# Optimization experiments

Measured on AMD Instinct MI355X. Metric: run time of the kernel, lower is better.

## Reference

```python
import jax, jax.numpy as jnp
import numpy as np

N = 50000      # n_nodes
E = 800000     # n_edges
F_IN = 128     # raw feature dim
H = 64         # hidden_channels
L = 2          # max_hash_hops / num GCN layers
NUM_PERM = 128 # minhash permutations
HLL_M = 64     # 2**hll_p registers


def setup_inputs() -> dict:
    key = jax.random.key(0)
    ks = jax.random.split(key, 8)
    x = jax.random.normal(ks[0], (N, F_IN), jnp.float32)
    edge_index = jax.random.randint(ks[1], (2, E), 0, N, dtype=jnp.int32)
    minhash0 = jax.random.randint(ks[2], (N, NUM_PERM), 0, 2147483647, dtype=jnp.int32)
    hll0 = jax.random.randint(ks[3], (N, HLL_M), 0, 20, dtype=jnp.int32)
    W_enc = jax.random.normal(ks[4], (F_IN, H), jnp.float32) / np.sqrt(F_IN)
    b_enc = jnp.zeros((H,), jnp.float32)
    W_convs = jax.random.normal(ks[5], (L, H, H), jnp.float32) / np.sqrt(H)
    b_convs = jnp.zeros((L, H), jnp.float32)
    return {"x": x, "edge_index": edge_index, "minhash0": minhash0, "hll0": hll0,
            "W_enc": W_enc, "b_enc": b_enc, "W_convs": W_convs, "b_convs": b_convs}


def _hll_count(hll):
    # standard HyperLogLog estimator: alpha_m * m^2 / sum(2^-reg)
    m = hll.shape[1]
    alpha = 0.7213 / (1.0 + 1.079 / m)
    s = jnp.sum(jnp.exp2(-hll.astype(jnp.float32)), axis=1)  # [N]
    return alpha * m * m / s


def reference(x, edge_index, minhash0, hll0, W_enc, b_enc, W_convs, b_convs):
    src, dst = edge_index[0], edge_index[1]
    loops = jnp.arange(N, dtype=src.dtype)
    # add_self_loops: used for both hash propagation and (internally) by GCNConv
    src_sl = jnp.concatenate([src, loops])  # [E+N]
    dst_sl = jnp.concatenate([dst, loops])

    # gcn_norm: D^-1/2 (A+I) D^-1/2 with degrees counted on self-looped graph
    deg = jax.ops.segment_sum(jnp.ones_like(dst_sl, jnp.float32), dst_sl, num_segments=N)
    dis = jnp.where(deg > 0, jax.lax.rsqrt(jnp.maximum(deg, 1.0)), 0.0)
    norm = dis[src_sl] * dis[dst_sl]  # [E+N]

    # k=0: feature encoder (dropout off in eval)
    h = x @ W_enc + b_enc  # [N, H]

    mh, hll = minhash0, hll0
    cards = []
    for k in range(L):
        # hash propagation: HLL = register-wise max over neighborhood,
        # minhash = permutation-wise min over neighborhood (self-looped graph)
        hll = jax.ops.segment_max(hll[src_sl], dst_sl, num_segments=N)
        mh = jax.ops.segment_min(mh[src_sl], dst_sl, num_segments=N)
        cards.append(_hll_count(hll))
        # GCNConv: gather - (x W) - scatter with symmetric norm, then residual
        msg = (h @ W_convs[k])[src_sl] * norm[:, None]  # [E+N, H]
        out = jax.ops.segment_sum(msg, dst_sl, num_segments=N) + b_convs[k]
        h = h + out  # feature_prop == 'residual' (dropout off)

    cards = jnp.stack(cards, axis=1)  # [N, L]
    return h, cards, mh, hll
```

## Files before the change

kernel.cpp:

```cpp
#include <hip/hip_runtime.h>
#include <hip/hip_bf16.h>

typedef unsigned int uint;
typedef unsigned short ushort;

#define N_NODES 50000
#define N_EDGES 800000
#define FDIM 128
#define HID 64
#define NPERM 128
#define HLLM 64

#define BSHIFT 8
#define BNODES 256
#define NBUCK 196
#define SCAT_BLOCKS 256
#define EDGES_PER_BLK 3125
#define HIST_BLOCKS 64
#define EDGES_PER_HIST 12500
#define MH_BLOCKS 12500
#define HLL_BLOCKS 3125
#define SLICE_CAP 6400
#define CONV_BLOCKS 782


__device__ __forceinline__ void mh_body(int node, int l, const int* __restrict__ offsets,
                                        const ushort* __restrict__ csr,
                                        const uint* __restrict__ mh_in,
                                        uint* __restrict__ out_p, float* __restrict__ out_f) {
    int s = offsets[node], e = offsets[node + 1];
    uint mn0 = 0xFFFFu, mn1 = 0xFFFFu, mn2 = 0xFFFFu, mn3 = 0xFFFFu;
    for (int p = s; p < e; p += 8) {
        int q1 = p + 1, q2 = p + 2, q3 = p + 3, q4 = p + 4, q5 = p + 5, q6 = p + 6, q7 = p + 7;
        uint j0 = csr[p];
        uint j1 = csr[q1 < e ? q1 : p];
        uint j2 = csr[q2 < e ? q2 : p];
        uint j3 = csr[q3 < e ? q3 : p];
        uint j4 = csr[q4 < e ? q4 : p];
        uint j5 = csr[q5 < e ? q5 : p];
        uint j6 = csr[q6 < e ? q6 : p];
        uint j7 = csr[q7 < e ? q7 : p];
        uint a0 = mh_in[(size_t)j0 * 64 + l];
        uint a1 = mh_in[(size_t)j1 * 64 + l];
        uint a2 = mh_in[(size_t)j2 * 64 + l];
        uint a3 = mh_in[(size_t)j3 * 64 + l];
        uint a4 = mh_in[(size_t)j4 * 64 + l];
        uint a5 = mh_in[(size_t)j5 * 64 + l];
        uint a6 = mh_in[(size_t)j6 * 64 + l];
        uint a7 = mh_in[(size_t)j7 * 64 + l];
        mn0 = min(mn0, min(a0 & 0xFFFFu, a1 & 0xFFFFu));
        mn1 = min(mn1, min(a0 >> 16, a1 >> 16));
        mn2 = min(mn2, min(a2 & 0xFFFFu, a3 & 0xFFFFu));
        mn3 = min(mn3, min(a2 >> 16, a3 >> 16));
        mn0 = min(mn0, min(a4 & 0xFFFFu, a5 & 0xFFFFu));
        mn1 = min(mn1, min(a4 >> 16, a5 >> 16));
        mn2 = min(mn2, min(a6 & 0xFFFFu, a7 & 0xFFFFu));
        mn3 = min(mn3, min(a6 >> 16, a7 >> 16));
    }
    mn0 = min(mn0, mn2); mn1 = min(mn1, mn3);
    if (out_p) {
        out_p[(size_t)node * 64 + l] = mn0 | (mn1 << 16);
    } else {
        float2 w;
        w.x = __uint_as_float(mn0 << 16);
        w.y = __uint_as_float(mn1 << 16);
        *(float2*)(out_f + (size_t)node * NPERM + 2 * l) = w;
    }
}

__device__ __forceinline__ void hll_body(int node, int q, const int* __restrict__ offsets,
                                         const ushort* __restrict__ csr,
                                         const uint* __restrict__ hll_in,
                                         uint* __restrict__ out_p, float* __restrict__ out_f,
                                         float* __restrict__ cards, int kcol) {
    int s = offsets[node], e = offsets[node + 1];
    uint m0 = 0, m1 = 0, m2 = 0, m3 = 0;
#define HLL_ACC(vv) do { uint _v = (vv); \
        m0 = max(m0, _v & 0xFFu); m1 = max(m1, (_v >> 8) & 0xFFu); \
        m2 = max(m2, (_v >> 16) & 0xFFu); m3 = max(m3, _v >> 24); } while (0)
    for (int p = s; p < e; p += 8) {
        int q1 = p + 1, q2 = p + 2, q3 = p + 3, q4 = p + 4, q5 = p + 5, q6 = p + 6, q7 = p + 7;
        uint j0 = csr[p];
        uint j1 = csr[q1 < e ? q1 : p];
        uint j2 = csr[q2 < e ? q2 : p];
        uint j3 = csr[q3 < e ? q3 : p];
        uint j4 = csr[q4 < e ? q4 : p];
        uint j5 = csr[q5 < e ? q5 : p];
        uint j6 = csr[q6 < e ? q6 : p];
        uint j7 = csr[q7 < e ? q7 : p];
        uint a0 = hll_in[(size_t)j0 * 16 + q];
        uint a1 = hll_in[(size_t)j1 * 16 + q];
        uint a2 = hll_in[(size_t)j2 * 16 + q];
        uint a3 = hll_in[(size_t)j3 * 16 + q];
        uint a4 = hll_in[(size_t)j4 * 16 + q];
        uint a5 = hll_in[(size_t)j5 * 16 + q];
        uint a6 = hll_in[(size_t)j6 * 16 + q];
        uint a7 = hll_in[(size_t)j7 * 16 + q];
        HLL_ACC(a0); HLL_ACC(a1); HLL_ACC(a2); HLL_ACC(a3);
        HLL_ACC(a4); HLL_ACC(a5); HLL_ACC(a6); HLL_ACC(a7);
    }
#undef HLL_ACC
    if (out_p) out_p[(size_t)node * 16 + q] = m0 | (m1 << 8) | (m2 << 16) | (m3 << 24);
    if (out_f) {
        float4 w = {(float)m0, (float)m1, (float)m2, (float)m3};
        *(float4*)(out_f + (size_t)node * HLLM + 4 * q) = w;
    }
    float v = exp2f(-(float)m0) + exp2f(-(float)m1) + exp2f(-(float)m2) + exp2f(-(float)m3);
    v += __shfl_xor(v, 1); v += __shfl_xor(v, 2);
    v += __shfl_xor(v, 4); v += __shfl_xor(v, 8);
    if (q == 0) {
        const float alphamm = (float)(0.7213 / (1.0 + 1.079 / 64.0) * 64.0 * 64.0);
        cards[(size_t)node * 2 + kcol] = alphamm / v;
    }
}

__device__ __forceinline__ void agg_body(int node, int c, const int* __restrict__ offsets,
                                         const ushort* __restrict__ csr,
                                         const ushort* __restrict__ hWs,
                                         const float* __restrict__ dis,
                                         const float* __restrict__ b,
                                         const float* __restrict__ h_in,
                                         float* __restrict__ h_out) {
    int s = offsets[node], e = offsets[node + 1];
    float acc0 = 0.f, acc1 = 0.f;
    for (int p = s; p < e; p += 8) {
        int q1 = p + 1, q2 = p + 2, q3 = p + 3, q4 = p + 4, q5 = p + 5, q6 = p + 6, q7 = p + 7;
        bool v1 = q1 < e, v2 = q2 < e, v3 = q3 < e, v4 = q4 < e, v5 = q5 < e, v6 = q6 < e, v7 = q7 < e;
        uint j0 = csr[p];
        uint j1 = csr[v1 ? q1 : p];
        uint j2 = csr[v2 ? q2 : p];
        uint j3 = csr[v3 ? q3 : p];
        uint j4 = csr[v4 ? q4 : p];
        uint j5 = csr[v5 ? q5 : p];
        uint j6 = csr[v6 ? q6 : p];
        uint j7 = csr[v7 ? q7 : p];
        uint a0 = hWs[(size_t)j0 * HID + c];
        uint a1 = hWs[(size_t)j1 * HID + c];
        uint a2 = hWs[(size_t)j2 * HID + c];
        uint a3 = hWs[(size_t)j3 * HID + c];
        uint a4 = hWs[(size_t)j4 * HID + c];
        uint a5 = hWs[(size_t)j5 * HID + c];
        uint a6 = hWs[(size_t)j6 * HID + c];
        uint a7 = hWs[(size_t)j7 * HID + c];
        acc0 += __uint_as_float(a0 << 16);
        acc0 += v1 ? __uint_as_float(a1 << 16) : 0.f;
        acc1 += v2 ? __uint_as_float(a2 << 16) : 0.f;
        acc1 += v3 ? __uint_as_float(a3 << 16) : 0.f;
        acc0 += v4 ? __uint_as_float(a4 << 16) : 0.f;
        acc0 += v5 ? __uint_as_float(a5 << 16) : 0.f;
        acc1 += v6 ? __uint_as_float(a6 << 16) : 0.f;
        acc1 += v7 ? __uint_as_float(a7 << 16) : 0.f;
    }
    float acc = acc0 + acc1;
    h_out[(size_t)node * HID + c] = h_in[(size_t)node * HID + c] + b[c] + dis[node] * acc;
}

__device__ __forceinline__ void convmm_body(int row, int c0, const float* __restrict__ h,
                                            const float* __restrict__ Ws,
                                            const float* __restrict__ dis,
                                            ushort* __restrict__ hWs) {
    float acc[16] = {0.f, 0.f, 0.f, 0.f, 0.f, 0.f, 0.f, 0.f,
                     0.f, 0.f, 0.f, 0.f, 0.f, 0.f, 0.f, 0.f};
    const float4* hr = (const float4*)(h + (size_t)row * HID);
    for (int k4 = 0; k4 < HID / 4; ++k4) {
        float4 hv = hr[k4];
        const float* wr = Ws + (k4 * 4) * HID + c0;
#pragma unroll
        for (int j = 0; j < 16; ++j) acc[j] = fmaf(hv.x, wr[j], acc[j]);
#pragma unroll
        for (int j = 0; j < 16; ++j) acc[j] = fmaf(hv.y, wr[HID + j], acc[j]);
#pragma unroll
        for (int j = 0; j < 16; ++j) acc[j] = fmaf(hv.z, wr[2 * HID + j], acc[j]);
#pragma unroll
        for (int j = 0; j < 16; ++j) acc[j] = fmaf(hv.w, wr[3 * HID + j], acc[j]);
    }
    float d = dis[row];
    ushort* o = hWs + (size_t)row * HID + c0;
#pragma unroll
    for (int j = 0; j < 16; ++j) {
        __hip_bfloat16 t = __float2bfloat16(d * acc[j]);
        o[j] = *(ushort*)&t;
    }
}


__global__ void __launch_bounds__(256) k_prep(const float* __restrict__ x,
                       const float* __restrict__ W_enc, const float* __restrict__ b_enc,
                       float* __restrict__ h,
                       const int* __restrict__ mh, uint* __restrict__ mhp,
                       const int* __restrict__ hll, uint* __restrict__ hp,
                       const int* __restrict__ dst, int* __restrict__ hist2d) {
    __shared__ float smem[FDIM * HID];
    int b = blockIdx.x;
    if (b < CONV_BLOCKS) {
        for (int idx = threadIdx.x; idx < FDIM * HID; idx += 256) smem[idx] = W_enc[idx];
        __syncthreads();
        int row = b * 64 + (threadIdx.x >> 2);
        int c0 = (threadIdx.x & 3) * 16;
        if (row >= N_NODES) return;
        float acc[16];
#pragma unroll
        for (int j = 0; j < 16; ++j) acc[j] = b_enc[c0 + j];
        const float4* xr = (const float4*)(x + (size_t)row * FDIM);
        for (int k4 = 0; k4 < FDIM / 4; ++k4) {
            float4 xv = xr[k4];
            const float* wr = smem + (k4 * 4) * HID + c0;
#pragma unroll
            for (int j = 0; j < 16; ++j) acc[j] = fmaf(xv.x, wr[j], acc[j]);
#pragma unroll
            for (int j = 0; j < 16; ++j) acc[j] = fmaf(xv.y, wr[HID + j], acc[j]);
#pragma unroll
            for (int j = 0; j < 16; ++j) acc[j] = fmaf(xv.z, wr[2 * HID + j], acc[j]);
#pragma unroll
            for (int j = 0; j < 16; ++j) acc[j] = fmaf(xv.w, wr[3 * HID + j], acc[j]);
        }
        float* hr = h + (size_t)row * HID + c0;
#pragma unroll
        for (int j = 0; j < 16; ++j) hr[j] = acc[j];
    } else if (b < CONV_BLOCKS + MH_BLOCKS) {
        int i = (b - CONV_BLOCKS) * 256 + threadIdx.x;
        int2 v = ((const int2*)mh)[i];
        uint u0 = __float_as_uint((float)v.x) >> 16;
        uint u1 = __float_as_uint((float)v.y) >> 16;
        mhp[i] = u0 | (u1 << 16);
    } else if (b < CONV_BLOCKS + MH_BLOCKS + HLL_BLOCKS) {
        int i = (b - CONV_BLOCKS - MH_BLOCKS) * 256 + threadIdx.x;
        int4 v = ((const int4*)hll)[i];
        hp[i] = (uint)v.x | ((uint)v.y << 8) | ((uint)v.z << 16) | ((uint)v.w << 24);
    } else {
        int hb = b - CONV_BLOCKS - MH_BLOCKS - HLL_BLOCKS;
        int* hsh = (int*)smem;
        for (int i = threadIdx.x; i < NBUCK; i += 256) hsh[i] = 0;
        __syncthreads();
        int e0 = hb * EDGES_PER_HIST;
        for (int i = threadIdx.x; i < EDGES_PER_HIST; i += 256)
            atomicAdd(&hsh[dst[e0 + i] >> BSHIFT], 1);
        __syncthreads();
        for (int i = threadIdx.x; i < NBUCK; i += 256)
            hist2d[hb * NBUCK + i] = hsh[i];
    }
}

__global__ void k_bktscan(const int* __restrict__ hist2d, int* __restrict__ bktcnt,
                          int* __restrict__ gbase, int* __restrict__ gcur,
                          int* __restrict__ offsets) {
    __shared__ int s[256];
    int t = threadIdx.x;
    int v = 0;
    if (t < NBUCK)
        for (int k = 0; k < HIST_BLOCKS; ++k) v += hist2d[k * NBUCK + t];
    s[t] = v;
    __syncthreads();
    for (int off = 1; off < 256; off <<= 1) {
        int u = (t >= off) ? s[t - off] : 0;
        __syncthreads();
        s[t] += u;
        __syncthreads();
    }
    if (t < NBUCK) {
        int ex = s[t] - v;
        bktcnt[t] = v; gbase[t] = ex; gcur[t] = ex;
    }
    if (t == 0) offsets[N_NODES] = N_EDGES + N_NODES;
}


__global__ void __launch_bounds__(256) k_scatter(const int* __restrict__ src,
                          const int* __restrict__ dst,
                          int* __restrict__ gcur, uint* __restrict__ ebuf) {
    __shared__ uint ecache[EDGES_PER_BLK];
    __shared__ int cnt[NBUCK];
    __shared__ int cur[NBUCK];
    int t = threadIdx.x;
    for (int i = t; i < NBUCK; i += 256) cnt[i] = 0;
    __syncthreads();
    int e0 = blockIdx.x * EDGES_PER_BLK;
    for (int i = t; i < EDGES_PER_BLK; i += 256) {
        int d = dst[e0 + i];
        int s = src[e0 + i];
        ecache[i] = ((uint)s << 16) | (uint)d;
        atomicAdd(&cnt[d >> BSHIFT], 1);
    }
    __syncthreads();
    for (int b = t; b < NBUCK; b += 256)
        cur[b] = atomicAdd(&gcur[b], cnt[b]);
    __syncthreads();
    for (int i = t; i < EDGES_PER_BLK; i += 256) {
        uint en = ecache[i];
        uint d = en & 0xFFFFu;
        int p = atomicAdd(&cur[d >> BSHIFT], 1);
        ebuf[p] = ((en >> 16) << BSHIFT) | (d & (BNODES - 1));
    }
}


__global__ void __launch_bounds__(256) k_csr(const uint* __restrict__ ebuf,
                      const int* __restrict__ gbase, const int* __restrict__ bktcnt,
                      int* __restrict__ offsets, float* __restrict__ dis,
                      ushort* __restrict__ csr) {
    __shared__ int lcur[BNODES];
    __shared__ int ssum[256];
    __shared__ uint slice[SLICE_CAP];
    int b = blockIdx.x;
    int lo = b << BSHIFT;
    int nbkt = min(BNODES, N_NODES - lo);
    int ebase = gbase[b];
    int ecnt = bktcnt[b];
    int t = threadIdx.x;
    lcur[t] = 0;
    __syncthreads();
    for (int i = t; i < ecnt; i += 256)
        atomicAdd(&lcur[ebuf[ebase + i] & (BNODES - 1)], 1);
    __syncthreads();
    int a0 = lcur[t];
    ssum[t] = a0;
    __syncthreads();
    for (int off = 1; off < 256; off <<= 1) {
        int u = (t >= off) ? ssum[t - off] : 0;
        __syncthreads();
        ssum[t] += u;
        __syncthreads();
    }
    int pre = ssum[t] - a0;
    if (t < nbkt) {
        int st = pre + t;
        slice[st] = (uint)(lo + t);
        lcur[t] = st + 1;
        offsets[lo + t] = ebase + lo + st;
        dis[lo + t] = rsqrtf((float)(a0 + 1));
    }
    __syncthreads();
    for (int i = t; i < ecnt; i += 256) {
        uint en = ebuf[ebase + i];
        int p = atomicAdd(&lcur[en & (BNODES - 1)], 1);
        slice[p] = en >> BSHIFT;
    }
    __syncthreads();
    int slen = ecnt + nbkt;
    int gb = ebase + lo;
    for (int i = t; i < slen; i += 256) csr[gb + i] = (ushort)slice[i];
}


__global__ void __launch_bounds__(256) k_hopA(const int* __restrict__ offsets,
                    const ushort* __restrict__ csr,
                    const uint* __restrict__ mh_in, uint* __restrict__ mh_out_p,
                    const uint* __restrict__ hll_in, uint* __restrict__ hll_out_p,
                    float* __restrict__ cards,
                    const float* __restrict__ h, const float* __restrict__ W,
                    const float* __restrict__ dis, ushort* __restrict__ hWs) {
    __shared__ float Ws[HID * HID];
    int blk = blockIdx.x;
    if (blk < MH_BLOCKS) {
        int node = blk * 4 + (threadIdx.x >> 6);
        mh_body(node, threadIdx.x & 63, offsets, csr, mh_in, mh_out_p, nullptr);
    } else if (blk < MH_BLOCKS + HLL_BLOCKS) {
        int node = (blk - MH_BLOCKS) * 16 + (threadIdx.x >> 4);
        hll_body(node, threadIdx.x & 15, offsets, csr, hll_in, hll_out_p, nullptr, cards, 0);
    } else {
        for (int i = threadIdx.x; i < HID * HID; i += 256) Ws[i] = W[i];
        __syncthreads();
        int row = (blk - MH_BLOCKS - HLL_BLOCKS) * 64 + (threadIdx.x >> 2);
        if (row >= N_NODES) return;
        convmm_body(row, (threadIdx.x & 3) * 16, h, Ws, dis, hWs);
    }
}


__global__ void __launch_bounds__(256) k_hopB(const int* __restrict__ offsets,
                    const ushort* __restrict__ csr,
                    const uint* __restrict__ mh_in, float* __restrict__ mh_out_f,
                    const ushort* __restrict__ hWs, const float* __restrict__ b0,
                    float* __restrict__ h_cur,
                    const uint* __restrict__ hll_in, float* __restrict__ hll_out_f,
                    float* __restrict__ cards, const float* __restrict__ dis) {
    int blk = blockIdx.x;
    if (blk < MH_BLOCKS) {
        int node = blk * 4 + (threadIdx.x >> 6);
        mh_body(node, threadIdx.x & 63, offsets, csr, mh_in, nullptr, mh_out_f);
    } else if (blk < 2 * MH_BLOCKS) {
        int node = (blk - MH_BLOCKS) * 4 + (threadIdx.x >> 6);
        agg_body(node, threadIdx.x & 63, offsets, csr, hWs, dis, b0, h_cur, h_cur);
    } else {
        int node = (blk - 2 * MH_BLOCKS) * 16 + (threadIdx.x >> 4);
        hll_body(node, threadIdx.x & 15, offsets, csr, hll_in, nullptr, hll_out_f, cards, 1);
    }
}


__global__ void __launch_bounds__(256) k_conv(const float* __restrict__ h,
                         const float* __restrict__ W, const float* __restrict__ dis,
                         ushort* __restrict__ hWs) {
    __shared__ float Ws[HID * HID];
    for (int i = threadIdx.x; i < HID * HID; i += 256) Ws[i] = W[i];
    __syncthreads();
    int row = blockIdx.x * 64 + (threadIdx.x >> 2);
    if (row >= N_NODES) return;
    convmm_body(row, (threadIdx.x & 3) * 16, h, Ws, dis, hWs);
}


__global__ void __launch_bounds__(256) k_agg(const int* __restrict__ offsets,
                      const ushort* __restrict__ csr, const ushort* __restrict__ hWs,
                      const float* __restrict__ dis, const float* __restrict__ b,
                      const float* __restrict__ h_in, float* __restrict__ h_out) {
    int node = blockIdx.x * 4 + (threadIdx.x >> 6);
    agg_body(node, threadIdx.x & 63, offsets, csr, hWs, dis, b, h_in, h_out);
}


static inline char* align256(char* p) {
    return (char*)(((uintptr_t)p + 255) & ~(uintptr_t)255);
}

extern "C" void kernel_launch(void* const* d_in, const int* in_sizes, int n_in,
                              void* d_out, int out_size, void* d_ws, size_t ws_size,
                              hipStream_t stream) {
    const float* x       = (const float*)d_in[0];
    const int*   ei      = (const int*)d_in[1];
    const int*   mh0     = (const int*)d_in[2];
    const int*   hll0    = (const int*)d_in[3];
    const float* W_enc   = (const float*)d_in[4];
    const float* b_enc   = (const float*)d_in[5];
    const float* W_convs = (const float*)d_in[6];
    const float* b_convs = (const float*)d_in[7];

    float* out       = (float*)d_out;
    float* out_h     = out;
    float* out_cards = out + (size_t)N_NODES * HID;
    float* out_mh    = out_cards + (size_t)N_NODES * 2;
    float* out_hll   = out_mh + (size_t)N_NODES * NPERM;

    char* w = (char*)d_ws;
    int*   hist2d  = (int*)w;   w = align256(w + (size_t)HIST_BLOCKS * NBUCK * 4);
    int*   bktcnt  = (int*)w;   w = align256(w + (size_t)NBUCK * 4);
    int*   gbase   = (int*)w;   w = align256(w + (size_t)NBUCK * 4);
    int*   gcur    = (int*)w;   w = align256(w + (size_t)NBUCK * 4);
    int*   offsets = (int*)w;   w = align256(w + (size_t)(N_NODES + 1) * 4);
    float* dis     = (float*)w; w = align256(w + (size_t)N_NODES * 4);
    ushort* csr    = (ushort*)w; w = align256(w + (size_t)(N_EDGES + N_NODES) * 2);
    uint*  mhp0    = (uint*)w;  w = align256(w + (size_t)N_NODES * 64 * 4);
    uint*  mhA     = (uint*)w;  w = align256(w + (size_t)N_NODES * 64 * 4);
    uint*  hp0     = (uint*)w;  w = align256(w + (size_t)N_NODES * 16 * 4);
    uint*  hllA    = (uint*)w;  w = align256(w + (size_t)N_NODES * 16 * 4);
    float* h_cur   = (float*)w; w = align256(w + (size_t)N_NODES * HID * 4);
    ushort* hWs    = (ushort*)w; w = align256(w + (size_t)N_NODES * HID * 2);
    uint*  ebuf    = mhA;

    const int* src = ei;
    const int* dst = ei + N_EDGES;

    k_prep<<<CONV_BLOCKS + MH_BLOCKS + HLL_BLOCKS + HIST_BLOCKS, 256, 0, stream>>>(
        x, W_enc, b_enc, h_cur, mh0, mhp0, hll0, hp0, dst, hist2d);
    k_bktscan<<<1, 256, 0, stream>>>(hist2d, bktcnt, gbase, gcur, offsets);
    k_scatter<<<SCAT_BLOCKS, 256, 0, stream>>>(src, dst, gcur, ebuf);
    k_csr<<<NBUCK, 256, 0, stream>>>(ebuf, gbase, bktcnt, offsets, dis, csr);

    k_hopA<<<MH_BLOCKS + HLL_BLOCKS + CONV_BLOCKS, 256, 0, stream>>>(
        offsets, csr, mhp0, mhA, hp0, hllA, out_cards, h_cur, W_convs, dis, hWs);
    k_hopB<<<2 * MH_BLOCKS + HLL_BLOCKS, 256, 0, stream>>>(
        offsets, csr, mhA, out_mh, hWs, b_convs, h_cur, hllA, out_hll, out_cards, dis);
    k_conv<<<CONV_BLOCKS, 256, 0, stream>>>(h_cur, W_convs + HID * HID, dis, hWs);
    k_agg<<<MH_BLOCKS, 256, 0, stream>>>(offsets, csr, hWs, dis, b_convs + HID, h_cur, out_h);
}
```

Measured before the change: 215.6 us.

## Pad CSR rows to multiples of eight with dummy node for vector index loads

```diff
diff --git a/kernel.cpp b/kernel.cpp
--- a/kernel.cpp
+++ b/kernel.cpp
@@ -10,6 +10,7 @@
 #define HID 64
 #define NPERM 128
 #define HLLM 64
+#define DUMMY 50000
 
 #define BSHIFT 8
 #define BNODES 256
@@ -20,44 +21,43 @@
 #define EDGES_PER_HIST 12500
 #define MH_BLOCKS 12500
 #define HLL_BLOCKS 3125
-#define SLICE_CAP 6400
+#define SLICE_CAP 8448
 #define CONV_BLOCKS 782
 
-
-__device__ __forceinline__ void mh_body(int node, int l, const int* __restrict__ offsets,
+__device__ __forceinline__ uint pk_min_u16(uint a, uint b) {
+    uint d;
+    asm("v_pk_min_u16 %0, %1, %2" : "=v"(d) : "v"(a), "v"(b));
+    return d;
+}
+
+
+__device__ __forceinline__ void mh_body(int node, uint l, const int2* __restrict__ off2,
                                         const ushort* __restrict__ csr,
                                         const uint* __restrict__ mh_in,
                                         uint* __restrict__ out_p, float* __restrict__ out_f) {
-    int s = offsets[node], e = offsets[node + 1];
-    uint mn0 = 0xFFFFu, mn1 = 0xFFFFu, mn2 = 0xFFFFu, mn3 = 0xFFFFu;
-    for (int p = s; p < e; p += 8) {
-        int q1 = p + 1, q2 = p + 2, q3 = p + 3, q4 = p + 4, q5 = p + 5, q6 = p + 6, q7 = p + 7;
-        uint j0 = csr[p];
-        uint j1 = csr[q1 < e ? q1 : p];
-        uint j2 = csr[q2 < e ? q2 : p];
-        uint j3 = csr[q3 < e ? q3 : p];
-        uint j4 = csr[q4 < e ? q4 : p];
-        uint j5 = csr[q5 < e ? q5 : p];
-        uint j6 = csr[q6 < e ? q6 : p];
-        uint j7 = csr[q7 < e ? q7 : p];
-        uint a0 = mh_in[(size_t)j0 * 64 + l];
-        uint a1 = mh_in[(size_t)j1 * 64 + l];
-        uint a2 = mh_in[(size_t)j2 * 64 + l];
-        uint a3 = mh_in[(size_t)j3 * 64 + l];
-        uint a4 = mh_in[(size_t)j4 * 64 + l];
-        uint a5 = mh_in[(size_t)j5 * 64 + l];
-        uint a6 = mh_in[(size_t)j6 * 64 + l];
-        uint a7 = mh_in[(size_t)j7 * 64 + l];
-        mn0 = min(mn0, min(a0 & 0xFFFFu, a1 & 0xFFFFu));
-        mn1 = min(mn1, min(a0 >> 16, a1 >> 16));
-        mn2 = min(mn2, min(a2 & 0xFFFFu, a3 & 0xFFFFu));
-        mn3 = min(mn3, min(a2 >> 16, a3 >> 16));
-        mn0 = min(mn0, min(a4 & 0xFFFFu, a5 & 0xFFFFu));
-        mn1 = min(mn1, min(a4 >> 16, a5 >> 16));
-        mn2 = min(mn2, min(a6 & 0xFFFFu, a7 & 0xFFFFu));
-        mn3 = min(mn3, min(a6 >> 16, a7 >> 16));
-    }
-    mn0 = min(mn0, mn2); mn1 = min(mn1, mn3);
+    int2 se = off2[node];
+    uint mnA = 0xFFFFFFFFu, mnB = 0xFFFFFFFFu, mnC = 0xFFFFFFFFu, mnD = 0xFFFFFFFFu;
+    for (int p = se.x; p < se.y; p += 8) {
+        uint4 c4 = *(const uint4*)(csr + p);
+        uint j0 = c4.x & 0xFFFFu, j1 = c4.x >> 16;
+        uint j2 = c4.y & 0xFFFFu, j3 = c4.y >> 16;
+        uint j4 = c4.z & 0xFFFFu, j5 = c4.z >> 16;
+        uint j6 = c4.w & 0xFFFFu, j7 = c4.w >> 16;
+        uint a0 = mh_in[j0 * 64u + l];
+        uint a1 = mh_in[j1 * 64u + l];
+        uint a2 = mh_in[j2 * 64u + l];
+        uint a3 = mh_in[j3 * 64u + l];
+        uint a4 = mh_in[j4 * 64u + l];
+        uint a5 = mh_in[j5 * 64u + l];
+        uint a6 = mh_in[j6 * 64u + l];
+        uint a7 = mh_in[j7 * 64u + l];
+        mnA = pk_min_u16(mnA, a0); mnB = pk_min_u16(mnB, a1);
+        mnC = pk_min_u16(mnC, a2); mnD = pk_min_u16(mnD, a3);
+        mnA = pk_min_u16(mnA, a4); mnB = pk_min_u16(mnB, a5);
+        mnC = pk_min_u16(mnC, a6); mnD = pk_min_u16(mnD, a7);
+    }
+    mnA = pk_min_u16(pk_min_u16(mnA, mnB), pk_min_u16(mnC, mnD));
+    uint mn0 = mnA & 0xFFFFu, mn1 = mnA >> 16;
     if (out_p) {
         out_p[(size_t)node * 64 + l] = mn0 | (mn1 << 16);
     } else {
@@ -68,34 +68,30 @@
     }
 }
 
-__device__ __forceinline__ void hll_body(int node, int q, const int* __restrict__ offsets,
+__device__ __forceinline__ void hll_body(int node, uint q, const int2* __restrict__ off2,
                                          const ushort* __restrict__ csr,
                                          const uint* __restrict__ hll_in,
                                          uint* __restrict__ out_p, float* __restrict__ out_f,
                                          float* __restrict__ cards, int kcol) {
-    int s = offsets[node], e = offsets[node + 1];
+    int2 se = off2[node];
     uint m0 = 0, m1 = 0, m2 = 0, m3 = 0;
 #define HLL_ACC(vv) do { uint _v = (vv); \
         m0 = max(m0, _v & 0xFFu); m1 = max(m1, (_v >> 8) & 0xFFu); \
         m2 = max(m2, (_v >> 16) & 0xFFu); m3 = max(m3, _v >> 24); } while (0)
-    for (int p = s; p < e; p += 8) {
-        int q1 = p + 1, q2 = p + 2, q3 = p + 3, q4 = p + 4, q5 = p + 5, q6 = p + 6, q7 = p + 7;
-        uint j0 = csr[p];
-        uint j1 = csr[q1 < e ? q1 : p];
-        uint j2 = csr[q2 < e ? q2 : p];
-        uint j3 = csr[q3 < e ? q3 : p];
-        uint j4 = csr[q4 < e ? q4 : p];
-        uint j5 = csr[q5 < e ? q5 : p];
-        uint j6 = csr[q6 < e ? q6 : p];
-        uint j7 = csr[q7 < e ? q7 : p];
-        uint a0 = hll_in[(size_t)j0 * 16 + q];
-        uint a1 = hll_in[(size_t)j1 * 16 + q];
-        uint a2 = hll_in[(size_t)j2 * 16 + q];
-        uint a3 = hll_in[(size_t)j3 * 16 + q];
-        uint a4 = hll_in[(size_t)j4 * 16 + q];
-        uint a5 = hll_in[(size_t)j5 * 16 + q];
-        uint a6 = hll_in[(size_t)j6 * 16 + q];
-        uint a7 = hll_in[(size_t)j7 * 16 + q];
+    for (int p = se.x; p < se.y; p += 8) {
+        uint4 c4 = *(const uint4*)(csr + p);
+        uint j0 = c4.x & 0xFFFFu, j1 = c4.x >> 16;
+        uint j2 = c4.y & 0xFFFFu, j3 = c4.y >> 16;
+        uint j4 = c4.z & 0xFFFFu, j5 = c4.z >> 16;
+        uint j6 = c4.w & 0xFFFFu, j7 = c4.w >> 16;
+        uint a0 = hll_in[j0 * 16u + q];
+        uint a1 = hll_in[j1 * 16u + q];
+        uint a2 = hll_in[j2 * 16u + q];
+        uint a3 = hll_in[j3 * 16u + q];
+        uint a4 = hll_in[j4 * 16u + q];
+        uint a5 = hll_in[j5 * 16u + q];
+        uint a6 = hll_in[j6 * 16u + q];
+        uint a7 = hll_in[j7 * 16u + q];
         HLL_ACC(a0); HLL_ACC(a1); HLL_ACC(a2); HLL_ACC(a3);
         HLL_ACC(a4); HLL_ACC(a5); HLL_ACC(a6); HLL_ACC(a7);
     }
@@ -114,42 +110,33 @@
     }
 }
 
-__device__ __forceinline__ void agg_body(int node, int c, const int* __restrict__ offsets,
+__device__ __forceinline__ void agg_body(int node, uint c, const int2* __restrict__ off2,
                                          const ushort* __restrict__ csr,
                                          const ushort* __restrict__ hWs,
                                          const float* __restrict__ dis,
                                          const float* __restrict__ b,
                                          const float* __restrict__ h_in,
                                          float* __restrict__ h_out) {
-    int s = offsets[node], e = offsets[node + 1];
+    int2 se = off2[node];
     float acc0 = 0.f, acc1 = 0.f;
-    for (int p = s; p < e; p += 8) {
-        int q1 = p + 1, q2 = p + 2, q3 = p + 3, q4 = p + 4, q5 = p + 5, q6 = p + 6, q7 = p + 7;
-        bool v1 = q1 < e, v2 = q2 < e, v3 = q3 < e, v4 = q4 < e, v5 = q5 < e, v6 = q6 < e, v7 = q7 < e;
-        uint j0 = csr[p];
-        uint j1 = csr[v1 ? q1 : p];
-        uint j2 = csr[v2 ? q2 : p];
-        uint j3 = csr[v3 ? q3 : p];
-        uint j4 = csr[v4 ? q4 : p];
-        uint j5 = csr[v5 ? q5 : p];
-        uint j6 = csr[v6 ? q6 : p];
-        uint j7 = csr[v7 ? q7 : p];
-        uint a0 = hWs[(size_t)j0 * HID + c];
-        uint a1 = hWs[(size_t)j1 * HID + c];
-        uint a2 = hWs[(size_t)j2 * HID + c];
-        uint a3 = hWs[(size_t)j3 * HID + c];
-        uint a4 = hWs[(size_t)j4 * HID + c];
-        uint a5 = hWs[(size_t)j5 * HID + c];
-        uint a6 = hWs[(size_t)j6 * HID + c];
-        uint a7 = hWs[(size_t)j7 * HID + c];
-        acc0 += __uint_as_float(a0 << 16);
-        acc0 += v1 ? __uint_as_float(a1 << 16) : 0.f;
-        acc1 += v2 ? __uint_as_float(a2 << 16) : 0.f;
-        acc1 += v3 ? __uint_as_float(a3 << 16) : 0.f;
-        acc0 += v4 ? __uint_as_float(a4 << 16) : 0.f;
-        acc0 += v5 ? __uint_as_float(a5 << 16) : 0.f;
-        acc1 += v6 ? __uint_as_float(a6 << 16) : 0.f;
-        acc1 += v7 ? __uint_as_float(a7 << 16) : 0.f;
+    for (int p = se.x; p < se.y; p += 8) {
+        uint4 c4 = *(const uint4*)(csr + p);
+        uint j0 = c4.x & 0xFFFFu, j1 = c4.x >> 16;
+        uint j2 = c4.y & 0xFFFFu, j3 = c4.y >> 16;
+        uint j4 = c4.z & 0xFFFFu, j5 = c4.z >> 16;
+        uint j6 = c4.w & 0xFFFFu, j7 = c4.w >> 16;
+        uint a0 = hWs[j0 * 64u + c];
+        uint a1 = hWs[j1 * 64u + c];
+        uint a2 = hWs[j2 * 64u + c];
+        uint a3 = hWs[j3 * 64u + c];
+        uint a4 = hWs[j4 * 64u + c];
+        uint a5 = hWs[j5 * 64u + c];
+        uint a6 = hWs[j6 * 64u + c];
+        uint a7 = hWs[j7 * 64u + c];
+        acc0 += __uint_as_float(a0 << 16) + __uint_as_float(a1 << 16)
+              + __uint_as_float(a2 << 16) + __uint_as_float(a3 << 16);
+        acc1 += __uint_as_float(a4 << 16) + __uint_as_float(a5 << 16)
+              + __uint_as_float(a6 << 16) + __uint_as_float(a7 << 16);
     }
     float acc = acc0 + acc1;
     h_out[(size_t)node * HID + c] = h_in[(size_t)node * HID + c] + b[c] + dis[node] * acc;
@@ -187,8 +174,8 @@
 __global__ void __launch_bounds__(256) k_prep(const float* __restrict__ x,
                        const float* __restrict__ W_enc, const float* __restrict__ b_enc,
                        float* __restrict__ h,
-                       const int* __restrict__ mh, uint* __restrict__ mhp,
-                       const int* __restrict__ hll, uint* __restrict__ hp,
+                       const int* __restrict__ mh, uint* __restrict__ mhp, uint* __restrict__ mhA,
+                       const int* __restrict__ hll, uint* __restrict__ hp, uint* __restrict__ hllA,
                        const int* __restrict__ dst, int* __restrict__ hist2d) {
     __shared__ float smem[FDIM * HID];
     int b = blockIdx.x;
@@ -227,7 +214,7 @@
         int i = (b - CONV_BLOCKS - MH_BLOCKS) * 256 + threadIdx.x;
         int4 v = ((const int4*)hll)[i];
         hp[i] = (uint)v.x | ((uint)v.y << 8) | ((uint)v.z << 16) | ((uint)v.w << 24);
-    } else {
+    } else if (b < CONV_BLOCKS + MH_BLOCKS + HLL_BLOCKS + HIST_BLOCKS) {
         int hb = b - CONV_BLOCKS - MH_BLOCKS - HLL_BLOCKS;
         int* hsh = (int*)smem;
         for (int i = threadIdx.x; i < NBUCK; i += 256) hsh[i] = 0;
@@ -238,12 +225,22 @@
         __syncthreads();
         for (int i = threadIdx.x; i < NBUCK; i += 256)
             hist2d[hb * NBUCK + i] = hsh[i];
+    } else {
+        int t = threadIdx.x;
+        if (t < 64) {
+            mhp[(size_t)DUMMY * 64 + t] = 0xFFFFFFFFu;
+            mhA[(size_t)DUMMY * 64 + t] = 0xFFFFFFFFu;
+        } else if (t < 80) {
+            hp[(size_t)DUMMY * 16 + (t - 64)] = 0u;
+        } else if (t < 96) {
+            hllA[(size_t)DUMMY * 16 + (t - 80)] = 0u;
+        }
     }
 }
 
 __global__ void k_bktscan(const int* __restrict__ hist2d, int* __restrict__ bktcnt,
                           int* __restrict__ gbase, int* __restrict__ gcur,
-                          int* __restrict__ offsets) {
+                          int* __restrict__ pcur) {
     __shared__ int s[256];
     int t = threadIdx.x;
     int v = 0;
@@ -261,7 +258,7 @@
         int ex = s[t] - v;
         bktcnt[t] = v; gbase[t] = ex; gcur[t] = ex;
     }
-    if (t == 0) offsets[N_NODES] = N_EDGES + N_NODES;
+    if (t == 0) pcur[0] = 0;
 }
 
 
@@ -296,11 +293,12 @@
 
 __global__ void __launch_bounds__(256) k_csr(const uint* __restrict__ ebuf,
                       const int* __restrict__ gbase, const int* __restrict__ bktcnt,
-                      int* __restrict__ offsets, float* __restrict__ dis,
-                      ushort* __restrict__ csr) {
+                      int* __restrict__ pcur, int2* __restrict__ off2,
+                      float* __restrict__ dis, ushort* __restrict__ csr) {
     __shared__ int lcur[BNODES];
     __shared__ int ssum[256];
     __shared__ uint slice[SLICE_CAP];
+    __shared__ int sbase;
     int b = blockIdx.x;
     int lo = b << BSHIFT;
     int nbkt = min(BNODES, N_NODES - lo);
@@ -313,7 +311,8 @@
         atomicAdd(&lcur[ebuf[ebase + i] & (BNODES - 1)], 1);
     __syncthreads();
     int a0 = lcur[t];
-    ssum[t] = a0;
+    int plen = (t < nbkt) ? ((a0 + 8) & ~7) : 0;
+    ssum[t] = plen;
     __syncthreads();
     for (int off = 1; off < 256; off <<= 1) {
         int u = (t >= off) ? ssum[t - off] : 0;
@@ -321,12 +320,14 @@
         ssum[t] += u;
         __syncthreads();
     }
-    int pre = ssum[t] - a0;
+    int ppre = ssum[t] - plen;
+    if (t == 255) sbase = atomicAdd(pcur, ssum[255]);
+    __syncthreads();
+    int base = sbase;
     if (t < nbkt) {
-        int st = pre + t;
-        slice[st] = (uint)(lo + t);
-        lcur[t] = st + 1;
-        offsets[lo + t] = ebase + lo + st;
+        slice[ppre] = (uint)(lo + t);
+        lcur[t] = ppre + 1;
+        off2[lo + t] = make_int2(base + ppre, base + ppre + plen);
         dis[lo + t] = rsqrtf((float)(a0 + 1));
     }
     __syncthreads();
@@ -336,13 +337,15 @@
         slice[p] = en >> BSHIFT;
     }
     __syncthreads();
-    int slen = ecnt + nbkt;
-    int gb = ebase + lo;
-    for (int i = t; i < slen; i += 256) csr[gb + i] = (ushort)slice[i];
-}
-
-
-__global__ void __launch_bounds__(256) k_hopA(const int* __restrict__ offsets,
+    if (t < nbkt)
+        for (int i = lcur[t]; i < ppre + plen; ++i) slice[i] = DUMMY;
+    __syncthreads();
+    int total = ssum[255];
+    for (int i = t; i < total; i += 256) csr[base + i] = (ushort)slice[i];
+}
+
+
+__global__ void __launch_bounds__(256) k_hopA(const int2* __restrict__ off2,
                     const ushort* __restrict__ csr,
                     const uint* __restrict__ mh_in, uint* __restrict__ mh_out_p,
                     const uint* __restrict__ hll_in, uint* __restrict__ hll_out_p,
@@ -353,21 +356,28 @@
     int blk = blockIdx.x;
     if (blk < MH_BLOCKS) {
         int node = blk * 4 + (threadIdx.x >> 6);
-        mh_body(node, threadIdx.x & 63, offsets, csr, mh_in, mh_out_p, nullptr);
+        mh_body(node, threadIdx.x & 63, off2, csr, mh_in, mh_out_p, nullptr);
     } else if (blk < MH_BLOCKS + HLL_BLOCKS) {
         int node = (blk - MH_BLOCKS) * 16 + (threadIdx.x >> 4);
-        hll_body(node, threadIdx.x & 15, offsets, csr, hll_in, hll_out_p, nullptr, cards, 0);
+        hll_body(node, threadIdx.x & 15, off2, csr, hll_in, hll_out_p, nullptr, cards, 0);
     } else {
         for (int i = threadIdx.x; i < HID * HID; i += 256) Ws[i] = W[i];
         __syncthreads();
         int row = (blk - MH_BLOCKS - HLL_BLOCKS) * 64 + (threadIdx.x >> 2);
-        if (row >= N_NODES) return;
-        convmm_body(row, (threadIdx.x & 3) * 16, h, Ws, dis, hWs);
-    }
-}
-
-
-__global__ void __launch_bounds__(256) k_hopB(const int* __restrict__ offsets,
+        int c0 = (threadIdx.x & 3) * 16;
+        if (row > N_NODES) return;
+        if (row == N_NODES) {
+            ushort* o = hWs + (size_t)row * HID + c0;
+#pragma unroll
+            for (int j = 0; j < 16; ++j) o[j] = 0;
+            return;
+        }
+        convmm_body(row, c0, h, Ws, dis, hWs);
+    }
+}
+
+
+__global__ void __launch_bounds__(256) k_hopB(const int2* __restrict__ off2,
                     const ushort* __restrict__ csr,
                     const uint* __restrict__ mh_in, float* __restrict__ mh_out_f,
                     const ushort* __restrict__ hWs, const float* __restrict__ b0,
@@ -377,13 +387,13 @@
     int blk = blockIdx.x;
     if (blk < MH_BLOCKS) {
         int node = blk * 4 + (threadIdx.x >> 6);
-        mh_body(node, threadIdx.x & 63, offsets, csr, mh_in, nullptr, mh_out_f);
+        mh_body(node, threadIdx.x & 63, off2, csr, mh_in, nullptr, mh_out_f);
     } else if (blk < 2 * MH_BLOCKS) {
         int node = (blk - MH_BLOCKS) * 4 + (threadIdx.x >> 6);
-        agg_body(node, threadIdx.x & 63, offsets, csr, hWs, dis, b0, h_cur, h_cur);
+        agg_body(node, threadIdx.x & 63, off2, csr, hWs, dis, b0, h_cur, h_cur);
     } else {
         int node = (blk - 2 * MH_BLOCKS) * 16 + (threadIdx.x >> 4);
-        hll_body(node, threadIdx.x & 15, offsets, csr, hll_in, nullptr, hll_out_f, cards, 1);
+        hll_body(node, threadIdx.x & 15, off2, csr, hll_in, nullptr, hll_out_f, cards, 1);
     }
 }
 
@@ -395,17 +405,24 @@
     for (int i = threadIdx.x; i < HID * HID; i += 256) Ws[i] = W[i];
     __syncthreads();
     int row = blockIdx.x * 64 + (threadIdx.x >> 2);
-    if (row >= N_NODES) return;
-    convmm_body(row, (threadIdx.x & 3) * 16, h, Ws, dis, hWs);
-}
-
-
-__global__ void __launch_bounds__(256) k_agg(const int* __restrict__ offsets,
+    int c0 = (threadIdx.x & 3) * 16;
+    if (row > N_NODES) return;
+    if (row == N_NODES) {
+        ushort* o = hWs + (size_t)row * HID + c0;
+#pragma unroll
+        for (int j = 0; j < 16; ++j) o[j] = 0;
+        return;
+    }
+    convmm_body(row, c0, h, Ws, dis, hWs);
+}
+
+
+__global__ void __launch_bounds__(256) k_agg(const int2* __restrict__ off2,
                       const ushort* __restrict__ csr, const ushort* __restrict__ hWs,
                       const float* __restrict__ dis, const float* __restrict__ b,
                       const float* __restrict__ h_in, float* __restrict__ h_out) {
     int node = blockIdx.x * 4 + (threadIdx.x >> 6);
-    agg_body(node, threadIdx.x & 63, offsets, csr, hWs, dis, b, h_in, h_out);
+    agg_body(node, threadIdx.x & 63, off2, csr, hWs, dis, b, h_in, h_out);
 }
 
 
@@ -436,30 +453,31 @@
     int*   bktcnt  = (int*)w;   w = align256(w + (size_t)NBUCK * 4);
     int*   gbase   = (int*)w;   w = align256(w + (size_t)NBUCK * 4);
     int*   gcur    = (int*)w;   w = align256(w + (size_t)NBUCK * 4);
-    int*   offsets = (int*)w;   w = align256(w + (size_t)(N_NODES + 1) * 4);
+    int*   pcur    = (int*)w;   w = align256(w + 4);
+    int2*  off2    = (int2*)w;  w = align256(w + (size_t)N_NODES * 8);
     float* dis     = (float*)w; w = align256(w + (size_t)N_NODES * 4);
-    ushort* csr    = (ushort*)w; w = align256(w + (size_t)(N_EDGES + N_NODES) * 2);
-    uint*  mhp0    = (uint*)w;  w = align256(w + (size_t)N_NODES * 64 * 4);
-    uint*  mhA     = (uint*)w;  w = align256(w + (size_t)N_NODES * 64 * 4);
-    uint*  hp0     = (uint*)w;  w = align256(w + (size_t)N_NODES * 16 * 4);
-    uint*  hllA    = (uint*)w;  w = align256(w + (size_t)N_NODES * 16 * 4);
+    ushort* csr    = (ushort*)w; w = align256(w + (size_t)(N_EDGES + 8 * N_NODES) * 2);
+    uint*  mhp0    = (uint*)w;  w = align256(w + (size_t)(N_NODES + 1) * 64 * 4);
+    uint*  mhA     = (uint*)w;  w = align256(w + (size_t)(N_NODES + 1) * 64 * 4);
+    uint*  hp0     = (uint*)w;  w = align256(w + (size_t)(N_NODES + 1) * 16 * 4);
+    uint*  hllA    = (uint*)w;  w = align256(w + (size_t)(N_NODES + 1) * 16 * 4);
     float* h_cur   = (float*)w; w = align256(w + (size_t)N_NODES * HID * 4);
-    ushort* hWs    = (ushort*)w; w = align256(w + (size_t)N_NODES * HID * 2);
+    ushort* hWs    = (ushort*)w; w = align256(w + (size_t)(N_NODES + 1) * HID * 2);
     uint*  ebuf    = mhA;
 
     const int* src = ei;
     const int* dst = ei + N_EDGES;
 
-    k_prep<<<CONV_BLOCKS + MH_BLOCKS + HLL_BLOCKS + HIST_BLOCKS, 256, 0, stream>>>(
-        x, W_enc, b_enc, h_cur, mh0, mhp0, hll0, hp0, dst, hist2d);
-    k_bktscan<<<1, 256, 0, stream>>>(hist2d, bktcnt, gbase, gcur, offsets);
+    k_prep<<<CONV_BLOCKS + MH_BLOCKS + HLL_BLOCKS + HIST_BLOCKS + 1, 256, 0, stream>>>(
+        x, W_enc, b_enc, h_cur, mh0, mhp0, mhA, hll0, hp0, hllA, dst, hist2d);
+    k_bktscan<<<1, 256, 0, stream>>>(hist2d, bktcnt, gbase, gcur, pcur);
     k_scatter<<<SCAT_BLOCKS, 256, 0, stream>>>(src, dst, gcur, ebuf);
-    k_csr<<<NBUCK, 256, 0, stream>>>(ebuf, gbase, bktcnt, offsets, dis, csr);
-
-    k_hopA<<<MH_BLOCKS + HLL_BLOCKS + CONV_BLOCKS, 256, 0, stream>>>(
-        offsets, csr, mhp0, mhA, hp0, hllA, out_cards, h_cur, W_convs, dis, hWs);
+    k_csr<<<NBUCK, 256, 0, stream>>>(ebuf, gbase, bktcnt, pcur, off2, dis, csr);
+
+    k_hopA<<<MH_BLOCKS + HLL_BLOCKS + CONV_BLOCKS + 1, 256, 0, stream>>>(
+        off2, csr, mhp0, mhA, hp0, hllA, out_cards, h_cur, W_convs, dis, hWs);
     k_hopB<<<2 * MH_BLOCKS + HLL_BLOCKS, 256, 0, stream>>>(
-        offsets, csr, mhA, out_mh, hWs, b_convs, h_cur, hllA, out_hll, out_cards, dis);
-    k_conv<<<CONV_BLOCKS, 256, 0, stream>>>(h_cur, W_convs + HID * HID, dis, hWs);
-    k_agg<<<MH_BLOCKS, 256, 0, stream>>>(offsets, csr, hWs, dis, b_convs + HID, h_cur, out_h);
-}
+        off2, csr, mhA, out_mh, hWs, b_convs, h_cur, hllA, out_hll, out_cards, dis);
+    k_conv<<<CONV_BLOCKS + 1, 256, 0, stream>>>(h_cur, W_convs + HID * HID, dis, hWs);
+    k_agg<<<MH_BLOCKS, 256, 0, stream>>>(off2, csr, hWs, dis, b_convs + HID, h_cur, out_h);
+}
```

Result: faster. 211.0 us (-2.1%).
